# Kernel tuning notes

Hardware: AMD Instinct MI355X
Metric: run time of the kernel (lower is better)

## Reference

```python
import jax, jax.numpy as jnp
import numpy as np

N = 8192  # number of candidates being ranked


def setup_inputs() -> dict:
    key = jax.random.key(0)
    k1, k2 = jax.random.split(key)
    logits = jax.random.normal(k1, (N,), dtype=jnp.float32)
    rankings = jax.random.randint(k2, (N,), 0, N).astype(jnp.int64)
    return {"logits": logits, "rankings": rankings}


def reference(logits, rankings):
    # Vectorized WeightedRankNetLoss:
    #   loss = (1/N) * sum_{i<j, r_i<r_j} log(1 + exp(logits[j]-logits[i])) / (r_i + r_j)
    n = logits.shape[0]
    idx = jnp.arange(n)
    # pair selected iff i < j AND rankings[i] < rankings[j]
    pair_mask = (idx[:, None] < idx[None, :]) & (rankings[:, None] < rankings[None, :])
    r = rankings.astype(logits.dtype)
    rsum = r[:, None] + r[None, :]
    # For selected pairs r_j >= r_i + 1 >= 1, so rsum >= 1; clamp only protects masked entries.
    w = jnp.where(pair_mask, 1.0, 0.0) / jnp.maximum(rsum, 1.0)  # [N, N]
    d = logits[None, :] - logits[:, None]  # d[i, j] = logits[j] - logits[i]
    loss = jnp.sum(w * jax.nn.softplus(d))  # softplus = log(1+exp(.)), numerically stable
    return loss / n
```

## Files before the change

### kernel.cpp

```cpp
#include <hip/hip_runtime.h>

#define N_CAND 8192
#define TILE   64
#define NTILES (N_CAND / TILE)
#define NLIVE  (NTILES * (NTILES + 1) / 2)
#define WPB    16
#define NBLK   256
#define NWAVE  (NBLK * WPB)


__device__ __forceinline__ float fast_rcp(float x) {
    float y = __int_as_float(0x7EF311C3 - __float_as_int(x));
    y = y * fmaf(-x, y, 2.0f);
    y = y * fmaf(-x, y, 2.0f);
    return y;
}

__device__ __forceinline__ float tile_range_sum(
    const float* __restrict__ logits, const int* __restrict__ rankings,
    float* __restrict__ sEj, int* __restrict__ srj,
    int t, int lane, int j0, int j1)
{
    t = __builtin_amdgcn_readfirstlane(t);
    int bj = (int)((__builtin_sqrtf(8.0f * (float)t + 1.0f) - 1.0f) * 0.5f);
    while ((bj + 1) * (bj + 2) / 2 <= t) ++bj;
    while (bj * (bj + 1) / 2 > t)       --bj;
    const int bi = t - bj * (bj + 1) / 2;

    const float LOG2E = 1.4426950408889634f;

    const float lis = logits[bi * TILE + lane] * LOG2E;
    const int   ri  = rankings[bi * TILE + lane];
    const float ljs = logits[bj * TILE + lane] * LOG2E;
    const int   rj  = rankings[bj * TILE + lane];

    const float Ei = __builtin_amdgcn_exp2f(lis);
    sEj[lane] = __builtin_amdgcn_exp2f(ljs);
    srj[lane] = rj;

    float accL0 = 0.0f, accL1 = 0.0f, accL2 = 0.0f, accL3 = 0.0f;
    float accW0 = 0.0f, accW1 = 0.0f, accW2 = 0.0f, accW3 = 0.0f;

    if (bi != bj) {
        #pragma unroll 1
        for (int jj = j0; jj < j1; jj += 4) {
            const float Ej0 = sEj[jj    ], Ej1 = sEj[jj + 1];
            const float Ej2 = sEj[jj + 2], Ej3 = sEj[jj + 3];
            const int   rj0 = srj[jj    ], rj1 = srj[jj + 1];
            const int   rj2 = srj[jj + 2], rj3 = srj[jj + 3];

            const float L0 = __builtin_amdgcn_logf(Ei + Ej0);
            const float L1 = __builtin_amdgcn_logf(Ei + Ej1);
            const float L2 = __builtin_amdgcn_logf(Ei + Ej2);
            const float L3 = __builtin_amdgcn_logf(Ei + Ej3);

            const float u0 = fast_rcp((float)(ri + rj0));
            const float u1 = fast_rcp((float)(ri + rj1));
            const float u2 = fast_rcp((float)(ri + rj2));
            const float u3 = fast_rcp((float)(ri + rj3));

            const float w0 = (rj0 > ri) ? u0 : 0.0f;
            const float w1 = (rj1 > ri) ? u1 : 0.0f;
            const float w2 = (rj2 > ri) ? u2 : 0.0f;
            const float w3 = (rj3 > ri) ? u3 : 0.0f;

            accL0 = fmaf(w0, L0, accL0);  accW0 += w0;
            accL1 = fmaf(w1, L1, accL1);  accW1 += w1;
            accL2 = fmaf(w2, L2, accL2);  accW2 += w2;
            accL3 = fmaf(w3, L3, accL3);  accW3 += w3;
        }
    } else {
        #pragma unroll 1
        for (int jj = j0; jj < j1; jj += 4) {
            const float Ej0 = sEj[jj    ], Ej1 = sEj[jj + 1];
            const float Ej2 = sEj[jj + 2], Ej3 = sEj[jj + 3];
            const int   rj0 = srj[jj    ], rj1 = srj[jj + 1];
            const int   rj2 = srj[jj + 2], rj3 = srj[jj + 3];

            const float L0 = __builtin_amdgcn_logf(Ei + Ej0);
            const float L1 = __builtin_amdgcn_logf(Ei + Ej1);
            const float L2 = __builtin_amdgcn_logf(Ei + Ej2);
            const float L3 = __builtin_amdgcn_logf(Ei + Ej3);

            const float u0 = fast_rcp((float)(ri + rj0));
            const float u1 = fast_rcp((float)(ri + rj1));
            const float u2 = fast_rcp((float)(ri + rj2));
            const float u3 = fast_rcp((float)(ri + rj3));

            const float w0 = ((jj     > lane) && (rj0 > ri)) ? u0 : 0.0f;
            const float w1 = ((jj + 1 > lane) && (rj1 > ri)) ? u1 : 0.0f;
            const float w2 = ((jj + 2 > lane) && (rj2 > ri)) ? u2 : 0.0f;
            const float w3 = ((jj + 3 > lane) && (rj3 > ri)) ? u3 : 0.0f;

            accL0 = fmaf(w0, L0, accL0);  accW0 += w0;
            accL1 = fmaf(w1, L1, accL1);  accW1 += w1;
            accL2 = fmaf(w2, L2, accL2);  accW2 += w2;
            accL3 = fmaf(w3, L3, accL3);  accW3 += w3;
        }
    }

    const float accL = (accL0 + accL1) + (accL2 + accL3);
    const float accW = (accW0 + accW1) + (accW2 + accW3);
    return fmaf(-lis, accW, accL);
}

__global__ __launch_bounds__(1024, 4) void ranknet_fused_kernel(
    const float* __restrict__ logits,
    const int*   __restrict__ rankings,
    float*       __restrict__ out)
{
    __shared__ float s_Ej[WPB][TILE];
    __shared__ int   s_rj[WPB][TILE];
    __shared__ float s_w[WPB];

    const int tid  = threadIdx.x;
    const int lane = tid & 63;
    const int wave = tid >> 6;
    const int gw   = __builtin_amdgcn_readfirstlane((int)blockIdx.x * WPB + wave);

    float lacc = 0.0f;
    #pragma unroll 1
    for (int k = 0; k < 3; ++k) {
        int tt, jj0, jj1;
        bool live = true;
        if (k == 0)      { tt = gw;          jj0 = 0; jj1 = TILE; }
        else if (k == 1) { tt = gw + NWAVE;  jj0 = 0; jj1 = TILE; }
        else {
            const int c = gw >> 4;
            live = ((gw & 15) == (c & 3));
            tt   = 2 * NWAVE + (c >> 2);
            jj0  = (c & 3) * 16;
            jj1  = jj0 + 16;
        }
        if (live)
            lacc += tile_range_sum(logits, rankings, s_Ej[wave], s_rj[wave],
                                   tt, lane, jj0, jj1);
    }

    #pragma unroll
    for (int off = 32; off > 0; off >>= 1)
        lacc += __shfl_down(lacc, off, 64);
    if (lane == 0) s_w[wave] = lacc;
    __syncthreads();

    if (tid == 0) {
        float s = 0.0f;
        #pragma unroll
        for (int w = 0; w < WPB; ++w) s += s_w[w];
        const float LN2 = 0.6931471805599453f;
        atomicAdd(out, s * (LN2 / (float)N_CAND));
    }
}

extern "C" void kernel_launch(void* const* d_in, const int* in_sizes, int n_in,
                              void* d_out, int out_size, void* d_ws, size_t ws_size,
                              hipStream_t stream)
{
    const float* logits   = (const float*)d_in[0];
    const int*   rankings = (const int*)  d_in[1];
    float*       out      = (float*)d_out;
    (void)d_ws; (void)ws_size;

    ranknet_fused_kernel<<<dim3(NBLK), dim3(1024), 0, stream>>>(logits, rankings, out);
}
```

Before: 68.81 us.

## Precompute exp and float ranks in prep kernel; read j-tile via scalar loads

Adds a prep kernel that computes exp(logits) and float rankings once into workspace. The pair kernel then reads the j-tile directly from global memory with wave-uniform addresses instead of staging it through LDS, and fully unrolls the 64-wide inner loop via a DIAG template. The reciprocal drops to one Newton step and the int-to-float conversion leaves the inner loop. This trades a second kernel launch and lower reciprocal precision for fewer per-pair instructions and no LDS traffic.

```diff
diff --git a/kernel.cpp b/kernel.cpp
--- a/kernel.cpp
+++ b/kernel.cpp
@@ -9,137 +9,148 @@
 #define NWAVE  (NBLK * WPB)
 
 
-__device__ __forceinline__ float fast_rcp(float x) {
-    float y = __int_as_float(0x7EF311C3 - __float_as_int(x));
-    y = y * fmaf(-x, y, 2.0f);
-    y = y * fmaf(-x, y, 2.0f);
-    return y;
+__device__ __forceinline__ void decode_t(int t, int& bi, int& bj) {
+    int b = (int)((__builtin_sqrtf(8.0f * (float)t + 1.0f) - 1.0f) * 0.5f);
+    while ((b + 1) * (b + 2) / 2 <= t) ++b;
+    while (b * (b + 1) / 2 > t)       --b;
+    bj = b; bi = t - b * (b + 1) / 2;
 }
 
-__device__ __forceinline__ float tile_range_sum(
-    const float* __restrict__ logits, const int* __restrict__ rankings,
-    float* __restrict__ sEj, int* __restrict__ srj,
-    int t, int lane, int j0, int j1)
+__device__ __forceinline__ float rcp1(float x) {
+    float y = __int_as_float(0x7EF311C3 - __float_as_int(x));
+    return y * fmaf(-x, y, 2.0f);
+}
+
+template<bool DIAG>
+__device__ __forceinline__ float tile_sum64(
+    const float* __restrict__ E, const float* __restrict__ RF,
+    const float* __restrict__ logits,
+    int bi, int bj, int lane)
 {
-    t = __builtin_amdgcn_readfirstlane(t);
-    int bj = (int)((__builtin_sqrtf(8.0f * (float)t + 1.0f) - 1.0f) * 0.5f);
-    while ((bj + 1) * (bj + 2) / 2 <= t) ++bj;
-    while (bj * (bj + 1) / 2 > t)       --bj;
-    const int bi = t - bj * (bj + 1) / 2;
-
     const float LOG2E = 1.4426950408889634f;
-
     const float lis = logits[bi * TILE + lane] * LOG2E;
-    const int   ri  = rankings[bi * TILE + lane];
-    const float ljs = logits[bj * TILE + lane] * LOG2E;
-    const int   rj  = rankings[bj * TILE + lane];
-
-    const float Ei = __builtin_amdgcn_exp2f(lis);
-    sEj[lane] = __builtin_amdgcn_exp2f(ljs);
-    srj[lane] = rj;
+    const float rif = RF[bi * TILE + lane];
+    const float Ei  = E [bi * TILE + lane];
+    const float* __restrict__ jE = E  + bj * TILE;
+    const float* __restrict__ jR = RF + bj * TILE;
 
     float accL0 = 0.0f, accL1 = 0.0f, accL2 = 0.0f, accL3 = 0.0f;
     float accW0 = 0.0f, accW1 = 0.0f, accW2 = 0.0f, accW3 = 0.0f;
 
-    if (bi != bj) {
-        #pragma unroll 1
-        for (int jj = j0; jj < j1; jj += 4) {
-            const float Ej0 = sEj[jj    ], Ej1 = sEj[jj + 1];
-            const float Ej2 = sEj[jj + 2], Ej3 = sEj[jj + 3];
-            const int   rj0 = srj[jj    ], rj1 = srj[jj + 1];
-            const int   rj2 = srj[jj + 2], rj3 = srj[jj + 3];
+    #pragma unroll
+    for (int jj = 0; jj < TILE; jj += 4) {
+        const float Ej0 = jE[jj    ], rj0 = jR[jj    ];
+        const float Ej1 = jE[jj + 1], rj1 = jR[jj + 1];
+        const float Ej2 = jE[jj + 2], rj2 = jR[jj + 2];
+        const float Ej3 = jE[jj + 3], rj3 = jR[jj + 3];
 
-            const float L0 = __builtin_amdgcn_logf(Ei + Ej0);
-            const float L1 = __builtin_amdgcn_logf(Ei + Ej1);
-            const float L2 = __builtin_amdgcn_logf(Ei + Ej2);
-            const float L3 = __builtin_amdgcn_logf(Ei + Ej3);
+        const float L0 = __builtin_amdgcn_logf(Ei + Ej0);
+        const float L1 = __builtin_amdgcn_logf(Ei + Ej1);
+        const float L2 = __builtin_amdgcn_logf(Ei + Ej2);
+        const float L3 = __builtin_amdgcn_logf(Ei + Ej3);
 
-            const float u0 = fast_rcp((float)(ri + rj0));
-            const float u1 = fast_rcp((float)(ri + rj1));
-            const float u2 = fast_rcp((float)(ri + rj2));
-            const float u3 = fast_rcp((float)(ri + rj3));
+        const float u0 = rcp1(rif + rj0);
+        const float u1 = rcp1(rif + rj1);
+        const float u2 = rcp1(rif + rj2);
+        const float u3 = rcp1(rif + rj3);
 
-            const float w0 = (rj0 > ri) ? u0 : 0.0f;
-            const float w1 = (rj1 > ri) ? u1 : 0.0f;
-            const float w2 = (rj2 > ri) ? u2 : 0.0f;
-            const float w3 = (rj3 > ri) ? u3 : 0.0f;
+        bool s0 = (rj0 > rif), s1 = (rj1 > rif), s2 = (rj2 > rif), s3 = (rj3 > rif);
+        if (DIAG) {
+            s0 = s0 && (jj     > lane);
+            s1 = s1 && (jj + 1 > lane);
+            s2 = s2 && (jj + 2 > lane);
+            s3 = s3 && (jj + 3 > lane);
+        }
+        const float w0 = s0 ? u0 : 0.0f;
+        const float w1 = s1 ? u1 : 0.0f;
+        const float w2 = s2 ? u2 : 0.0f;
+        const float w3 = s3 ? u3 : 0.0f;
 
-            accL0 = fmaf(w0, L0, accL0);  accW0 += w0;
-            accL1 = fmaf(w1, L1, accL1);  accW1 += w1;
-            accL2 = fmaf(w2, L2, accL2);  accW2 += w2;
-            accL3 = fmaf(w3, L3, accL3);  accW3 += w3;
-        }
-    } else {
-        #pragma unroll 1
-        for (int jj = j0; jj < j1; jj += 4) {
-            const float Ej0 = sEj[jj    ], Ej1 = sEj[jj + 1];
-            const float Ej2 = sEj[jj + 2], Ej3 = sEj[jj + 3];
-            const int   rj0 = srj[jj    ], rj1 = srj[jj + 1];
-            const int   rj2 = srj[jj + 2], rj3 = srj[jj + 3];
-
-            const float L0 = __builtin_amdgcn_logf(Ei + Ej0);
-            const float L1 = __builtin_amdgcn_logf(Ei + Ej1);
-            const float L2 = __builtin_amdgcn_logf(Ei + Ej2);
-            const float L3 = __builtin_amdgcn_logf(Ei + Ej3);
-
-            const float u0 = fast_rcp((float)(ri + rj0));
-            const float u1 = fast_rcp((float)(ri + rj1));
-            const float u2 = fast_rcp((float)(ri + rj2));
-            const float u3 = fast_rcp((float)(ri + rj3));
-
-            const float w0 = ((jj     > lane) && (rj0 > ri)) ? u0 : 0.0f;
-            const float w1 = ((jj + 1 > lane) && (rj1 > ri)) ? u1 : 0.0f;
-            const float w2 = ((jj + 2 > lane) && (rj2 > ri)) ? u2 : 0.0f;
-            const float w3 = ((jj + 3 > lane) && (rj3 > ri)) ? u3 : 0.0f;
-
-            accL0 = fmaf(w0, L0, accL0);  accW0 += w0;
-            accL1 = fmaf(w1, L1, accL1);  accW1 += w1;
-            accL2 = fmaf(w2, L2, accL2);  accW2 += w2;
-            accL3 = fmaf(w3, L3, accL3);  accW3 += w3;
-        }
+        accL0 = fmaf(w0, L0, accL0);  accW0 += w0;
+        accL1 = fmaf(w1, L1, accL1);  accW1 += w1;
+        accL2 = fmaf(w2, L2, accL2);  accW2 += w2;
+        accL3 = fmaf(w3, L3, accL3);  accW3 += w3;
     }
 
-    const float accL = (accL0 + accL1) + (accL2 + accL3);
-    const float accW = (accW0 + accW1) + (accW2 + accW3);
+    const float aL = (accL0 + accL1) + (accL2 + accL3);
+    const float aW = (accW0 + accW1) + (accW2 + accW3);
+    return fmaf(-lis, aW, aL);
+}
+
+__device__ __forceinline__ float tile_sum_range(
+    const float* __restrict__ E, const float* __restrict__ RF,
+    const float* __restrict__ logits,
+    int bi, int bj, int lane, int j0, int j1)
+{
+    const float LOG2E = 1.4426950408889634f;
+    const float lis = logits[bi * TILE + lane] * LOG2E;
+    const float rif = RF[bi * TILE + lane];
+    const float Ei  = E [bi * TILE + lane];
+    const float* __restrict__ jE = E  + bj * TILE;
+    const float* __restrict__ jR = RF + bj * TILE;
+    const bool diag = (bi == bj);
+
+    float accL = 0.0f, accW = 0.0f;
+    #pragma unroll 1
+    for (int jj = j0; jj < j1; ++jj) {
+        const float Ej  = jE[jj];
+        const float rjf = jR[jj];
+        const float L   = __builtin_amdgcn_logf(Ei + Ej);
+        const float u   = rcp1(rif + rjf);
+        const bool  sel = (rjf > rif) && (!diag || jj > lane);
+        const float w   = sel ? u : 0.0f;
+        accL = fmaf(w, L, accL);  accW += w;
+    }
     return fmaf(-lis, accW, accL);
 }
 
-__global__ __launch_bounds__(1024, 4) void ranknet_fused_kernel(
+__global__ __launch_bounds__(256) void ranknet_prep_kernel(
     const float* __restrict__ logits,
     const int*   __restrict__ rankings,
+    float*       __restrict__ E,
+    float*       __restrict__ RF)
+{
+    const int i = blockIdx.x * 256 + threadIdx.x;
+    const float LOG2E = 1.4426950408889634f;
+    E [i] = __builtin_amdgcn_exp2f(logits[i] * LOG2E);
+    RF[i] = (float)rankings[i];
+}
+
+__global__ __launch_bounds__(1024, 4) void ranknet_pairs_kernel(
+    const float* __restrict__ logits,
+    const float* __restrict__ E,
+    const float* __restrict__ RF,
     float*       __restrict__ out)
 {
-    __shared__ float s_Ej[WPB][TILE];
-    __shared__ int   s_rj[WPB][TILE];
-    __shared__ float s_w[WPB];
-
     const int tid  = threadIdx.x;
     const int lane = tid & 63;
     const int wave = tid >> 6;
     const int gw   = __builtin_amdgcn_readfirstlane((int)blockIdx.x * WPB + wave);
 
     float lacc = 0.0f;
+
     #pragma unroll 1
-    for (int k = 0; k < 3; ++k) {
-        int tt, jj0, jj1;
-        bool live = true;
-        if (k == 0)      { tt = gw;          jj0 = 0; jj1 = TILE; }
-        else if (k == 1) { tt = gw + NWAVE;  jj0 = 0; jj1 = TILE; }
-        else {
-            const int c = gw >> 4;
-            live = ((gw & 15) == (c & 3));
-            tt   = 2 * NWAVE + (c >> 2);
-            jj0  = (c & 3) * 16;
-            jj1  = jj0 + 16;
+    for (int k = 0; k < 2; ++k) {
+        const int t = __builtin_amdgcn_readfirstlane(gw + k * NWAVE);
+        int bi, bj; decode_t(t, bi, bj);
+        if (bi == bj) lacc += tile_sum64<true >(E, RF, logits, bi, bj, lane);
+        else          lacc += tile_sum64<false>(E, RF, logits, bi, bj, lane);
+    }
+
+    {
+        const int c = gw >> 4;
+        if ((gw & 15) == (c & 3)) {
+            int bi, bj; decode_t(2 * NWAVE + (c >> 2), bi, bj);
+            const int j0 = (c & 3) * 16;
+            lacc += tile_sum_range(E, RF, logits, bi, bj, lane, j0, j0 + 16);
         }
-        if (live)
-            lacc += tile_range_sum(logits, rankings, s_Ej[wave], s_rj[wave],
-                                   tt, lane, jj0, jj1);
     }
 
     #pragma unroll
     for (int off = 32; off > 0; off >>= 1)
         lacc += __shfl_down(lacc, off, 64);
+
+    __shared__ float s_w[WPB];
     if (lane == 0) s_w[wave] = lacc;
     __syncthreads();
 
@@ -159,7 +170,9 @@
     const float* logits   = (const float*)d_in[0];
     const int*   rankings = (const int*)  d_in[1];
     float*       out      = (float*)d_out;
-    (void)d_ws; (void)ws_size;
+    float*       E        = (float*)d_ws;
+    float*       RF       = (float*)d_ws + N_CAND;
 
-    ranknet_fused_kernel<<<dim3(NBLK), dim3(1024), 0, stream>>>(logits, rankings, out);
+    ranknet_prep_kernel <<<dim3(N_CAND / 256), dim3(256), 0, stream>>>(logits, rankings, E, RF);
+    ranknet_pairs_kernel<<<dim3(NBLK), dim3(1024), 0, stream>>>(logits, E, RF, out);
 }
```

Result: no change. 69.74 us (+1.4%).
